# Kernel optimization log

Hardware: AMD Instinct MI355X
Metric: run time of the kernel (lower is better)

## Reference

```python
import jax, jax.numpy as jnp
import numpy as np

N_NODES = 50000
N_EDGES = 800000
D = 128


def _gcn_norm(edge_index, edge_weights, n_nodes):
    # PyG gcn_norm with add_self_loops=True, fill_value=1.0
    src = jnp.concatenate([edge_index[0], jnp.arange(n_nodes)])
    dst = jnp.concatenate([edge_index[1], jnp.arange(n_nodes)])
    w = jnp.concatenate([edge_weights, jnp.ones((n_nodes,), edge_weights.dtype)])
    deg = jax.ops.segment_sum(w, dst, num_segments=n_nodes)
    dinv = jnp.where(deg > 0, jax.lax.rsqrt(deg), 0.0)
    norm = dinv[src] * w * dinv[dst]  # [E + N]
    return src, dst, norm


def _gcn_conv(x, src, dst, norm, W, b, n_nodes):
    h = x @ W                                   # [N, F_out]
    msg = h[src] * norm[:, None]                # gather + scale, [E+N, F_out]
    out = jax.ops.segment_sum(msg, dst, num_segments=n_nodes)
    return out + b


def setup_inputs() -> dict:
    key = jax.random.key(0)
    ks = jax.random.split(key, 12)
    s = 1.0 / np.sqrt(D)
    return {
        "x": jax.random.normal(ks[0], (N_NODES, D), jnp.float32),
        "edge_index": jax.random.randint(ks[1], (2, N_EDGES), 0, N_NODES, jnp.int64),
        "edge_weights": jax.random.uniform(ks[2], (N_EDGES,), jnp.float32),
        "W1": jax.random.normal(ks[3], (D, D), jnp.float32) * s,
        "b1": jnp.zeros((D,), jnp.float32),
        "W2": jax.random.normal(ks[4], (D, D), jnp.float32) * s,
        "b2": jnp.zeros((D,), jnp.float32),
        "W3": jax.random.normal(ks[5], (D, D), jnp.float32) * s,
        "b3": jnp.zeros((D,), jnp.float32),
        "Wl": jax.random.normal(ks[6], (D, D), jnp.float32) * s,
        "bl": jnp.zeros((D,), jnp.float32),
    }


def reference(x, edge_index, edge_weights, W1, b1, W2, b2, W3, b3, Wl, bl):
    n = x.shape[0]
    src, dst, norm = _gcn_norm(edge_index, edge_weights, n)
    h = _gcn_conv(x, src, dst, norm, W1, b1, n)
    h = jax.nn.relu(h)
    h = _gcn_conv(h, src, dst, norm, W2, b2, n)
    h = jax.nn.relu(h)
    h = _gcn_conv(h, src, dst, norm, W3, b3, n)
    # final 'linear' activation entry == nn.Linear(out_size, out_size)
    return h @ Wl + bl
```

## Files before the change

kernel.cpp:

```cpp
#include <hip/hip_runtime.h>
#include <hip/hip_fp16.h>


#define D 128
#define FXS 16777216.0f

typedef __attribute__((ext_vector_type(8))) _Float16 half8;
typedef __attribute__((ext_vector_type(4))) float floatx4;

__global__ __launch_bounds__(256) void k_init(unsigned long long* packed, int N) {
    int i = blockIdx.x * 256 + threadIdx.x;
    if (i < N) packed[i] = 0ull;
}

__global__ __launch_bounds__(256) void k_edge_pass1(const int* __restrict__ dst,
                                                    const float* __restrict__ w,
                                                    unsigned long long* packed,
                                                    int* __restrict__ loc, int E) {
    int e = blockIdx.x * 256 + threadIdx.x;
    if (e < E) {
        int d = dst[e];
        unsigned long long add =
            (1ull << 32) | (unsigned long long)__float2uint_rn(w[e] * FXS);
        unsigned long long old = atomicAdd(&packed[d], add);
        loc[e] = (int)(old >> 32);
    }
}

__global__ __launch_bounds__(256) void k_dinv(const unsigned long long* __restrict__ packed,
                                              float* dinv, int* cnt, int N) {
    int i = blockIdx.x * 256 + threadIdx.x;
    if (i < N) {
        unsigned long long p = packed[i];
        float deg = 1.0f + (float)(unsigned int)(p & 0xffffffffull) * (1.0f / FXS);
        dinv[i] = rsqrtf(deg);
        cnt[i] = (int)(p >> 32);
    }
}

__device__ inline int block_exscan_256(int v) {
    int tid = threadIdx.x;
    int lane = tid & 63, wv = tid >> 6;
    int incl = v;
#pragma unroll
    for (int d = 1; d < 64; d <<= 1) {
        int n = __shfl_up(incl, d, 64);
        if (lane >= d) incl += n;
    }
    __shared__ int wsum[4];
    if (lane == 63) wsum[wv] = incl;
    __syncthreads();
    int woff = 0;
#pragma unroll
    for (int j = 0; j < 4; j++) woff += (j < wv) ? wsum[j] : 0;
    return woff + incl - v;
}

__global__ __launch_bounds__(256) void k_scan_a(const int* __restrict__ cnt,
                                                int* bsum, int N) {
    int i = blockIdx.x * 256 + threadIdx.x;
    int v = (i < N) ? cnt[i] : 0;
#pragma unroll
    for (int d = 32; d; d >>= 1) v += __shfl_down(v, d, 64);
    __shared__ int ws4[4];
    int lane = threadIdx.x & 63, wv = threadIdx.x >> 6;
    if (lane == 0) ws4[wv] = v;
    __syncthreads();
    if (threadIdx.x == 0) bsum[blockIdx.x] = ws4[0] + ws4[1] + ws4[2] + ws4[3];
}

__global__ __launch_bounds__(256) void k_scan_b(const int* __restrict__ bsum,
                                                int* boff, int nb) {
    int tid = threadIdx.x;
    int v = (tid < nb) ? bsum[tid] : 0;
    int ex = block_exscan_256(v);
    if (tid < nb) boff[tid] = ex;
}

__global__ __launch_bounds__(256) void k_scan_c(const int* __restrict__ cnt,
                                                const int* __restrict__ boff,
                                                int* rp, int N, int E) {
    int i = blockIdx.x * 256 + threadIdx.x;
    int v = (i < N) ? cnt[i] : 0;
    int ex = block_exscan_256(v);
    if (i < N) rp[i] = boff[blockIdx.x] + ex;
    if (i == 0) rp[N] = E;
}

__global__ __launch_bounds__(256) void k_fill(const int* __restrict__ ei,
                                              const float* __restrict__ w,
                                              const float* __restrict__ dinv,
                                              const int* __restrict__ rp,
                                              const int* __restrict__ loc,
                                              float2* ev, int E) {
    int e = blockIdx.x * 256 + threadIdx.x;
    if (e < E) {
        int s = ei[e];
        int d = ei[E + e];
        int p = rp[d] + loc[e];
        ev[p] = make_float2(__int_as_float(s), dinv[s] * w[e] * dinv[d]);
    }
}

template <bool A_IS_F32>
__global__ __launch_bounds__(256) void k_gemm_mfma(const void* __restrict__ Aptr,
                                                   const float* __restrict__ W,
                                                   const float* __restrict__ bias,
                                                   float* __restrict__ C32,
                                                   __half* __restrict__ C16, int N) {
    __shared__ _Float16 Wl[128][136];
    int tid = threadIdx.x;

#pragma unroll
    for (int j = 0; j < 64; j++) {
        int e = tid + j * 256;
        int k = e >> 7, n = e & 127;
        Wl[n][k] = (_Float16)W[e];
    }
    __syncthreads();

    int wave = tid >> 6, lane = tid & 63;
    int m = lane & 15, q = lane >> 4;
    int R0 = blockIdx.x * 128 + wave * 32;

    const float*   A32p = (const float*)Aptr;
    const __half*  A16p = (const __half*)Aptr;

    floatx4 acc[2][8];
#pragma unroll
    for (int rt = 0; rt < 2; rt++)
#pragma unroll
        for (int ct = 0; ct < 8; ct++) acc[rt][ct] = (floatx4){0.f, 0.f, 0.f, 0.f};

#pragma unroll
    for (int kk = 0; kk < 4; kk++) {
        half8 a[2];
#pragma unroll
        for (int rt = 0; rt < 2; rt++) {
            int row = R0 + rt * 16 + m;
            half8 t = {0, 0, 0, 0, 0, 0, 0, 0};
            if (row < N) {
                if (A_IS_F32) {
                    const float* p = &A32p[(size_t)row * 128 + kk * 32 + q * 8];
                    float4 f0 = *(const float4*)p;
                    float4 f1 = *(const float4*)(p + 4);
                    t[0] = (_Float16)f0.x; t[1] = (_Float16)f0.y;
                    t[2] = (_Float16)f0.z; t[3] = (_Float16)f0.w;
                    t[4] = (_Float16)f1.x; t[5] = (_Float16)f1.y;
                    t[6] = (_Float16)f1.z; t[7] = (_Float16)f1.w;
                } else {
                    t = *(const half8*)&A16p[(size_t)row * 128 + kk * 32 + q * 8];
                }
            }
            a[rt] = t;
        }
#pragma unroll
        for (int ct = 0; ct < 8; ct++) {
            half8 b = *(const half8*)&Wl[ct * 16 + m][kk * 32 + q * 8];
            acc[0][ct] = __builtin_amdgcn_mfma_f32_16x16x32_f16(a[0], b, acc[0][ct], 0, 0, 0);
            acc[1][ct] = __builtin_amdgcn_mfma_f32_16x16x32_f16(a[1], b, acc[1][ct], 0, 0, 0);
        }
    }

#pragma unroll
    for (int rt = 0; rt < 2; rt++) {
#pragma unroll
        for (int ct = 0; ct < 8; ct++) {
            int col = ct * 16 + m;
            float bcol = (bias != nullptr) ? bias[col] : 0.f;
#pragma unroll
            for (int r = 0; r < 4; r++) {
                int row = R0 + rt * 16 + q * 4 + r;
                if (row < N) {
                    float v = acc[rt][ct][r];
                    if (C16) C16[(size_t)row * 128 + col] = __float2half_rn(v);
                    if (C32) C32[(size_t)row * 128 + col] = v + bcol;
                }
            }
        }
    }
}

__global__ __launch_bounds__(256) void k_agg(const __half* __restrict__ h16,
                                             const int* __restrict__ rp,
                                             const float2* __restrict__ ev,
                                             const float* __restrict__ dinv,
                                             const float* __restrict__ bias,
                                             __half* __restrict__ out16,
                                             int N, int relu) {
    int wave = blockIdx.x * 4 + (threadIdx.x >> 6);
    if (wave >= N) return;
    int lane = threadIdx.x & 63;
    int g = lane >> 4;
    int sl = lane & 15;
    int i = wave;

    float acc[8];
#pragma unroll
    for (int j = 0; j < 8; j++) acc[j] = 0.f;

    int e0 = rp[i], e1 = rp[i + 1];
    int e = e0;

#define GFMA(Q, V)                                                        \
    {                                                                     \
        union { uint4 u; __half2 h2[4]; } U; U.u = (Q);                   \
        float2 f0 = __half22float2(U.h2[0]);                              \
        float2 f1 = __half22float2(U.h2[1]);                              \
        float2 f2 = __half22float2(U.h2[2]);                              \
        float2 f3 = __half22float2(U.h2[3]);                              \
        acc[0] = fmaf(V, f0.x, acc[0]); acc[1] = fmaf(V, f0.y, acc[1]);   \
        acc[2] = fmaf(V, f1.x, acc[2]); acc[3] = fmaf(V, f1.y, acc[3]);   \
        acc[4] = fmaf(V, f2.x, acc[4]); acc[5] = fmaf(V, f2.y, acc[5]);   \
        acc[6] = fmaf(V, f3.x, acc[6]); acc[7] = fmaf(V, f3.y, acc[7]);   \
    }

    for (; e + 16 <= e1; e += 16) {
        float2 pA = ev[e + g];
        float2 pB = ev[e + 4 + g];
        float2 pC = ev[e + 8 + g];
        float2 pD = ev[e + 12 + g];
        uint4 qA = *(const uint4*)&h16[(size_t)__float_as_int(pA.x) * D + sl * 8];
        uint4 qB = *(const uint4*)&h16[(size_t)__float_as_int(pB.x) * D + sl * 8];
        uint4 qC = *(const uint4*)&h16[(size_t)__float_as_int(pC.x) * D + sl * 8];
        uint4 qD = *(const uint4*)&h16[(size_t)__float_as_int(pD.x) * D + sl * 8];
        GFMA(qA, pA.y); GFMA(qB, pB.y); GFMA(qC, pC.y); GFMA(qD, pD.y);
    }
    if (e + 8 <= e1) {
        float2 pA = ev[e + g];
        float2 pB = ev[e + 4 + g];
        uint4 qA = *(const uint4*)&h16[(size_t)__float_as_int(pA.x) * D + sl * 8];
        uint4 qB = *(const uint4*)&h16[(size_t)__float_as_int(pB.x) * D + sl * 8];
        GFMA(qA, pA.y); GFMA(qB, pB.y);
        e += 8;
    }
    if (e + 4 <= e1) {
        float2 pA = ev[e + g];
        uint4 qA = *(const uint4*)&h16[(size_t)__float_as_int(pA.x) * D + sl * 8];
        GFMA(qA, pA.y);
        e += 4;
    }
    if (e + g < e1) {
        float2 pA = ev[e + g];
        uint4 qA = *(const uint4*)&h16[(size_t)__float_as_int(pA.x) * D + sl * 8];
        GFMA(qA, pA.y);
    }
#undef GFMA

#pragma unroll
    for (int j = 0; j < 8; j++) {
        acc[j] += __shfl_xor(acc[j], 16, 64);
        acc[j] += __shfl_xor(acc[j], 32, 64);
    }

    if (g == 0) {
        float di = dinv[i];
        float self = di * di;
        union { uint4 u; __half2 h2[4]; } S;
        S.u = *(const uint4*)&h16[(size_t)i * D + sl * 8];
        float2 s0 = __half22float2(S.h2[0]);
        float2 s1 = __half22float2(S.h2[1]);
        float2 s2 = __half22float2(S.h2[2]);
        float2 s3 = __half22float2(S.h2[3]);
        float4 b0 = *(const float4*)&bias[sl * 8];
        float4 b1 = *(const float4*)&bias[sl * 8 + 4];
        float o[8];
        o[0] = acc[0] + b0.x + self * s0.x;
        o[1] = acc[1] + b0.y + self * s0.y;
        o[2] = acc[2] + b0.z + self * s1.x;
        o[3] = acc[3] + b0.w + self * s1.y;
        o[4] = acc[4] + b1.x + self * s2.x;
        o[5] = acc[5] + b1.y + self * s2.y;
        o[6] = acc[6] + b1.z + self * s3.x;
        o[7] = acc[7] + b1.w + self * s3.y;
        if (relu) {
#pragma unroll
            for (int j = 0; j < 8; j++) o[j] = fmaxf(o[j], 0.f);
        }
        union { uint4 u; __half2 h2[4]; } O;
        O.h2[0] = __float22half2_rn(make_float2(o[0], o[1]));
        O.h2[1] = __float22half2_rn(make_float2(o[2], o[3]));
        O.h2[2] = __float22half2_rn(make_float2(o[4], o[5]));
        O.h2[3] = __float22half2_rn(make_float2(o[6], o[7]));
        *(uint4*)&out16[(size_t)i * D + sl * 8] = O.u;
    }
}

extern "C" void kernel_launch(void* const* d_in, const int* in_sizes, int n_in,
                              void* d_out, int out_size, void* d_ws, size_t ws_size,
                              hipStream_t stream) {
    const float* x  = (const float*)d_in[0];
    const int*   ei = (const int*)d_in[1];
    const float* ew = (const float*)d_in[2];
    const float* W1 = (const float*)d_in[3];
    const float* b1 = (const float*)d_in[4];
    const float* W2 = (const float*)d_in[5];
    const float* b2 = (const float*)d_in[6];
    const float* W3 = (const float*)d_in[7];
    const float* b3 = (const float*)d_in[8];
    const float* Wl = (const float*)d_in[9];
    const float* bl = (const float*)d_in[10];

    int N = in_sizes[0] / D;
    int E = in_sizes[2];

    char* ws = (char*)d_ws;
    size_t off = 0;
    auto alloc = [&](size_t bytes) {
        void* p = ws + off;
        off = (off + bytes + 255) & ~(size_t)255;
        return p;
    };
    unsigned long long* packed = (unsigned long long*)alloc((size_t)N * 8);
    float*  dinv = (float*)alloc((size_t)N * 4);
    int*    cnt  = (int*)  alloc((size_t)N * 4);
    int*    bsum = (int*)  alloc(1024);
    int*    boff = (int*)  alloc(1024);
    int*    rp   = (int*)  alloc((size_t)(N + 1) * 4);
    int*    loc  = (int*)  alloc((size_t)E * 4);
    float2* ev   = (float2*)alloc((size_t)E * 8);
    __half* y16  = (__half*)alloc((size_t)N * D * 2);
    __half* z16  = (__half*)alloc((size_t)N * D * 2);

    int nbN = (N + 255) / 256;
    int nbE = (E + 255) / 256;

    k_init<<<nbN, 256, 0, stream>>>(packed, N);
    k_edge_pass1<<<nbE, 256, 0, stream>>>(ei + E, ew, packed, loc, E);
    k_dinv<<<nbN, 256, 0, stream>>>(packed, dinv, cnt, N);
    k_scan_a<<<nbN, 256, 0, stream>>>(cnt, bsum, N);
    k_scan_b<<<1, 256, 0, stream>>>(bsum, boff, nbN);
    k_scan_c<<<nbN, 256, 0, stream>>>(cnt, boff, rp, N, E);
    k_fill<<<nbE, 256, 0, stream>>>(ei, ew, dinv, rp, loc, ev, E);

    int gg = (N + 127) / 128;
    int ga = (N + 3) / 4;

    k_gemm_mfma<true ><<<gg, 256, 0, stream>>>(x,   W1, nullptr, nullptr, y16, N);
    k_agg<<<ga, 256, 0, stream>>>(y16, rp, ev, dinv, b1, z16, N, 1);
    k_gemm_mfma<false><<<gg, 256, 0, stream>>>(z16, W2, nullptr, nullptr, y16, N);
    k_agg<<<ga, 256, 0, stream>>>(y16, rp, ev, dinv, b2, z16, N, 1);
    k_gemm_mfma<false><<<gg, 256, 0, stream>>>(z16, W3, nullptr, nullptr, y16, N);
    k_agg<<<ga, 256, 0, stream>>>(y16, rp, ev, dinv, b3, z16, N, 0);
    k_gemm_mfma<false><<<gg, 256, 0, stream>>>(z16, Wl, bl, (float*)d_out, nullptr, N);
}
```

Baseline: 309.8 us.

## Pack edges into 32-bit words and fold symmetric normalization into GEMM epilogue

Edge records shrink from an 8-byte (src, norm) pair to a 4-byte word holding a 17-bit source index and a 15-bit quantized weight. The per-edge dinv[s]*dinv[d] factor is factored out: each GEMM scales its output rows by dinv, and aggregation multiplies by dinv of the destination. Degree is now computed from the CSR in a separate kernel, and the count atomics use strided padding instead of a packed 64-bit atomic. This halves edge-list traffic in the three aggregation passes. The cost is weight precision, down to about 15 bits, and a hard limit of 131072 nodes.

After: 305.0 us. Within noise of the previous version (-1.5%).

```diff
diff --git a/kernel.cpp b/kernel.cpp
--- a/kernel.cpp
+++ b/kernel.cpp
@@ -3,38 +3,19 @@
 
 
 #define D 128
-#define FXS 16777216.0f
 
 typedef __attribute__((ext_vector_type(8))) _Float16 half8;
 typedef __attribute__((ext_vector_type(4))) float floatx4;
 
-__global__ __launch_bounds__(256) void k_init(unsigned long long* packed, int N) {
-    int i = blockIdx.x * 256 + threadIdx.x;
-    if (i < N) packed[i] = 0ull;
-}
+#define CNT_STRIDE 16
 
 __global__ __launch_bounds__(256) void k_edge_pass1(const int* __restrict__ dst,
-                                                    const float* __restrict__ w,
-                                                    unsigned long long* packed,
+                                                    unsigned int* __restrict__ cntp,
                                                     int* __restrict__ loc, int E) {
     int e = blockIdx.x * 256 + threadIdx.x;
     if (e < E) {
         int d = dst[e];
-        unsigned long long add =
-            (1ull << 32) | (unsigned long long)__float2uint_rn(w[e] * FXS);
-        unsigned long long old = atomicAdd(&packed[d], add);
-        loc[e] = (int)(old >> 32);
-    }
-}
-
-__global__ __launch_bounds__(256) void k_dinv(const unsigned long long* __restrict__ packed,
-                                              float* dinv, int* cnt, int N) {
-    int i = blockIdx.x * 256 + threadIdx.x;
-    if (i < N) {
-        unsigned long long p = packed[i];
-        float deg = 1.0f + (float)(unsigned int)(p & 0xffffffffull) * (1.0f / FXS);
-        dinv[i] = rsqrtf(deg);
-        cnt[i] = (int)(p >> 32);
+        loc[e] = (int)atomicAdd(&cntp[(size_t)d * CNT_STRIDE], 1u);
     }
 }
 
@@ -56,10 +37,10 @@
     return woff + incl - v;
 }
 
-__global__ __launch_bounds__(256) void k_scan_a(const int* __restrict__ cnt,
+__global__ __launch_bounds__(256) void k_scan_a(const unsigned int* __restrict__ cntp,
                                                 int* bsum, int N) {
     int i = blockIdx.x * 256 + threadIdx.x;
-    int v = (i < N) ? cnt[i] : 0;
+    int v = (i < N) ? (int)cntp[(size_t)i * CNT_STRIDE] : 0;
 #pragma unroll
     for (int d = 32; d; d >>= 1) v += __shfl_down(v, d, 64);
     __shared__ int ws4[4];
@@ -77,11 +58,11 @@
     if (tid < nb) boff[tid] = ex;
 }
 
-__global__ __launch_bounds__(256) void k_scan_c(const int* __restrict__ cnt,
+__global__ __launch_bounds__(256) void k_scan_c(const unsigned int* __restrict__ cntp,
                                                 const int* __restrict__ boff,
                                                 int* rp, int N, int E) {
     int i = blockIdx.x * 256 + threadIdx.x;
-    int v = (i < N) ? cnt[i] : 0;
+    int v = (i < N) ? (int)cntp[(size_t)i * CNT_STRIDE] : 0;
     int ex = block_exscan_256(v);
     if (i < N) rp[i] = boff[blockIdx.x] + ex;
     if (i == 0) rp[N] = E;
@@ -89,22 +70,36 @@
 
 __global__ __launch_bounds__(256) void k_fill(const int* __restrict__ ei,
                                               const float* __restrict__ w,
-                                              const float* __restrict__ dinv,
                                               const int* __restrict__ rp,
                                               const int* __restrict__ loc,
-                                              float2* ev, int E) {
+                                              unsigned int* __restrict__ ev, int E) {
     int e = blockIdx.x * 256 + threadIdx.x;
     if (e < E) {
         int s = ei[e];
         int d = ei[E + e];
         int p = rp[d] + loc[e];
-        ev[p] = make_float2(__int_as_float(s), dinv[s] * w[e] * dinv[d]);
+        unsigned int wq = (unsigned int)__float2uint_rn(w[e] * 32767.0f);
+        ev[p] = (wq << 17) | (unsigned int)s;
+    }
+}
+
+__global__ __launch_bounds__(256) void k_deg(const int* __restrict__ rp,
+                                             const unsigned int* __restrict__ ev,
+                                             float* __restrict__ dinv, int N) {
+    int i = blockIdx.x * 256 + threadIdx.x;
+    if (i < N) {
+        int e0 = rp[i], e1 = rp[i + 1];
+        float s = 0.f;
+        for (int e = e0; e < e1; e++)
+            s += (float)(ev[e] >> 17);
+        dinv[i] = rsqrtf(1.0f + s * (1.0f / 32767.0f));
     }
 }
 
 template <bool A_IS_F32>
 __global__ __launch_bounds__(256) void k_gemm_mfma(const void* __restrict__ Aptr,
                                                    const float* __restrict__ W,
+                                                   const float* __restrict__ dinv,
                                                    const float* __restrict__ bias,
                                                    float* __restrict__ C32,
                                                    __half* __restrict__ C16, int N) {
@@ -123,8 +118,8 @@
     int m = lane & 15, q = lane >> 4;
     int R0 = blockIdx.x * 128 + wave * 32;
 
-    const float*   A32p = (const float*)Aptr;
-    const __half*  A16p = (const __half*)Aptr;
+    const float*  A32p = (const float*)Aptr;
+    const __half* A16p = (const __half*)Aptr;
 
     floatx4 acc[2][8];
 #pragma unroll
@@ -165,25 +160,24 @@
 #pragma unroll
     for (int rt = 0; rt < 2; rt++) {
 #pragma unroll
-        for (int ct = 0; ct < 8; ct++) {
-            int col = ct * 16 + m;
-            float bcol = (bias != nullptr) ? bias[col] : 0.f;
-#pragma unroll
-            for (int r = 0; r < 4; r++) {
-                int row = R0 + rt * 16 + q * 4 + r;
-                if (row < N) {
-                    float v = acc[rt][ct][r];
-                    if (C16) C16[(size_t)row * 128 + col] = __float2half_rn(v);
-                    if (C32) C32[(size_t)row * 128 + col] = v + bcol;
-                }
+        for (int r = 0; r < 4; r++) {
+            int row = R0 + rt * 16 + q * 4 + r;
+            if (row >= N) continue;
+            float dv = (dinv != nullptr) ? dinv[row] : 1.0f;
+#pragma unroll
+            for (int ct = 0; ct < 8; ct++) {
+                int col = ct * 16 + m;
+                float v = acc[rt][ct][r] * dv;
+                if (C16) C16[(size_t)row * 128 + col] = __float2half_rn(v);
+                if (C32) C32[(size_t)row * 128 + col] = v + bias[col];
             }
         }
     }
 }
 
-__global__ __launch_bounds__(256) void k_agg(const __half* __restrict__ h16,
+__global__ __launch_bounds__(256) void k_agg(const __half* __restrict__ y16,
                                              const int* __restrict__ rp,
-                                             const float2* __restrict__ ev,
+                                             const unsigned int* __restrict__ ev,
                                              const float* __restrict__ dinv,
                                              const float* __restrict__ bias,
                                              __half* __restrict__ out16,
@@ -214,37 +208,45 @@
         acc[4] = fmaf(V, f2.x, acc[4]); acc[5] = fmaf(V, f2.y, acc[5]);   \
         acc[6] = fmaf(V, f3.x, acc[6]); acc[7] = fmaf(V, f3.y, acc[7]);   \
     }
+#define UNPK(P, C, V)                                                     \
+    int   C = (int)((P) & 0x1FFFFu);                                      \
+    float V = (float)((P) >> 17) * (1.0f / 32767.0f);
 
     for (; e + 16 <= e1; e += 16) {
-        float2 pA = ev[e + g];
-        float2 pB = ev[e + 4 + g];
-        float2 pC = ev[e + 8 + g];
-        float2 pD = ev[e + 12 + g];
-        uint4 qA = *(const uint4*)&h16[(size_t)__float_as_int(pA.x) * D + sl * 8];
-        uint4 qB = *(const uint4*)&h16[(size_t)__float_as_int(pB.x) * D + sl * 8];
-        uint4 qC = *(const uint4*)&h16[(size_t)__float_as_int(pC.x) * D + sl * 8];
-        uint4 qD = *(const uint4*)&h16[(size_t)__float_as_int(pD.x) * D + sl * 8];
-        GFMA(qA, pA.y); GFMA(qB, pB.y); GFMA(qC, pC.y); GFMA(qD, pD.y);
+        unsigned int pA = ev[e + g];
+        unsigned int pB = ev[e + 4 + g];
+        unsigned int pC = ev[e + 8 + g];
+        unsigned int pD = ev[e + 12 + g];
+        UNPK(pA, cA, vA); UNPK(pB, cB, vB); UNPK(pC, cC, vC); UNPK(pD, cD, vD);
+        uint4 qA = *(const uint4*)&y16[(size_t)cA * D + sl * 8];
+        uint4 qB = *(const uint4*)&y16[(size_t)cB * D + sl * 8];
+        uint4 qC = *(const uint4*)&y16[(size_t)cC * D + sl * 8];
+        uint4 qD = *(const uint4*)&y16[(size_t)cD * D + sl * 8];
+        GFMA(qA, vA); GFMA(qB, vB); GFMA(qC, vC); GFMA(qD, vD);
     }
     if (e + 8 <= e1) {
-        float2 pA = ev[e + g];
-        float2 pB = ev[e + 4 + g];
-        uint4 qA = *(const uint4*)&h16[(size_t)__float_as_int(pA.x) * D + sl * 8];
-        uint4 qB = *(const uint4*)&h16[(size_t)__float_as_int(pB.x) * D + sl * 8];
-        GFMA(qA, pA.y); GFMA(qB, pB.y);
+        unsigned int pA = ev[e + g];
+        unsigned int pB = ev[e + 4 + g];
+        UNPK(pA, cA, vA); UNPK(pB, cB, vB);
+        uint4 qA = *(const uint4*)&y16[(size_t)cA * D + sl * 8];
+        uint4 qB = *(const uint4*)&y16[(size_t)cB * D + sl * 8];
+        GFMA(qA, vA); GFMA(qB, vB);
         e += 8;
     }
     if (e + 4 <= e1) {
-        float2 pA = ev[e + g];
-        uint4 qA = *(const uint4*)&h16[(size_t)__float_as_int(pA.x) * D + sl * 8];
-        GFMA(qA, pA.y);
+        unsigned int pA = ev[e + g];
+        UNPK(pA, cA, vA);
+        uint4 qA = *(const uint4*)&y16[(size_t)cA * D + sl * 8];
+        GFMA(qA, vA);
         e += 4;
     }
     if (e + g < e1) {
-        float2 pA = ev[e + g];
-        uint4 qA = *(const uint4*)&h16[(size_t)__float_as_int(pA.x) * D + sl * 8];
-        GFMA(qA, pA.y);
-    }
+        unsigned int pA = ev[e + g];
+        UNPK(pA, cA, vA);
+        uint4 qA = *(const uint4*)&y16[(size_t)cA * D + sl * 8];
+        GFMA(qA, vA);
+    }
+#undef UNPK
 #undef GFMA
 
 #pragma unroll
@@ -255,9 +257,8 @@
 
     if (g == 0) {
         float di = dinv[i];
-        float self = di * di;
         union { uint4 u; __half2 h2[4]; } S;
-        S.u = *(const uint4*)&h16[(size_t)i * D + sl * 8];
+        S.u = *(const uint4*)&y16[(size_t)i * D + sl * 8];
         float2 s0 = __half22float2(S.h2[0]);
         float2 s1 = __half22float2(S.h2[1]);
         float2 s2 = __half22float2(S.h2[2]);
@@ -265,14 +266,14 @@
         float4 b0 = *(const float4*)&bias[sl * 8];
         float4 b1 = *(const float4*)&bias[sl * 8 + 4];
         float o[8];
-        o[0] = acc[0] + b0.x + self * s0.x;
-        o[1] = acc[1] + b0.y + self * s0.y;
-        o[2] = acc[2] + b0.z + self * s1.x;
-        o[3] = acc[3] + b0.w + self * s1.y;
-        o[4] = acc[4] + b1.x + self * s2.x;
-        o[5] = acc[5] + b1.y + self * s2.y;
-        o[6] = acc[6] + b1.z + self * s3.x;
-        o[7] = acc[7] + b1.w + self * s3.y;
+        o[0] = b0.x + di * (acc[0] + s0.x);
+        o[1] = b0.y + di * (acc[1] + s0.y);
+        o[2] = b0.z + di * (acc[2] + s1.x);
+        o[3] = b0.w + di * (acc[3] + s1.y);
+        o[4] = b1.x + di * (acc[4] + s2.x);
+        o[5] = b1.y + di * (acc[5] + s2.y);
+        o[6] = b1.z + di * (acc[6] + s3.x);
+        o[7] = b1.w + di * (acc[7] + s3.y);
         if (relu) {
 #pragma unroll
             for (int j = 0; j < 8; j++) o[j] = fmaxf(o[j], 0.f);
@@ -311,36 +312,35 @@
         off = (off + bytes + 255) & ~(size_t)255;
         return p;
     };
-    unsigned long long* packed = (unsigned long long*)alloc((size_t)N * 8);
+    unsigned int* cntp = (unsigned int*)alloc((size_t)N * CNT_STRIDE * 4);
     float*  dinv = (float*)alloc((size_t)N * 4);
-    int*    cnt  = (int*)  alloc((size_t)N * 4);
     int*    bsum = (int*)  alloc(1024);
     int*    boff = (int*)  alloc(1024);
     int*    rp   = (int*)  alloc((size_t)(N + 1) * 4);
     int*    loc  = (int*)  alloc((size_t)E * 4);
-    float2* ev   = (float2*)alloc((size_t)E * 8);
+    unsigned int* ev = (unsigned int*)alloc((size_t)E * 4);
     __half* y16  = (__half*)alloc((size_t)N * D * 2);
     __half* z16  = (__half*)alloc((size_t)N * D * 2);
 
     int nbN = (N + 255) / 256;
     int nbE = (E + 255) / 256;
 
-    k_init<<<nbN, 256, 0, stream>>>(packed, N);
-    k_edge_pass1<<<nbE, 256, 0, stream>>>(ei + E, ew, packed, loc, E);
-    k_dinv<<<nbN, 256, 0, stream>>>(packed, dinv, cnt, N);
-    k_scan_a<<<nbN, 256, 0, stream>>>(cnt, bsum, N);
+    hipMemsetAsync(cntp, 0, (size_t)N * CNT_STRIDE * 4, stream);
+    k_edge_pass1<<<nbE, 256, 0, stream>>>(ei + E, cntp, loc, E);
+    k_scan_a<<<nbN, 256, 0, stream>>>(cntp, bsum, N);
     k_scan_b<<<1, 256, 0, stream>>>(bsum, boff, nbN);
-    k_scan_c<<<nbN, 256, 0, stream>>>(cnt, boff, rp, N, E);
-    k_fill<<<nbE, 256, 0, stream>>>(ei, ew, dinv, rp, loc, ev, E);
+    k_scan_c<<<nbN, 256, 0, stream>>>(cntp, boff, rp, N, E);
+    k_fill<<<nbE, 256, 0, stream>>>(ei, ew, rp, loc, ev, E);
+    k_deg<<<nbN, 256, 0, stream>>>(rp, ev, dinv, N);
 
     int gg = (N + 127) / 128;
     int ga = (N + 3) / 4;
 
-    k_gemm_mfma<true ><<<gg, 256, 0, stream>>>(x,   W1, nullptr, nullptr, y16, N);
+    k_gemm_mfma<true ><<<gg, 256, 0, stream>>>(x,   W1, dinv, nullptr, nullptr, y16, N);
     k_agg<<<ga, 256, 0, stream>>>(y16, rp, ev, dinv, b1, z16, N, 1);
-    k_gemm_mfma<false><<<gg, 256, 0, stream>>>(z16, W2, nullptr, nullptr, y16, N);
+    k_gemm_mfma<false><<<gg, 256, 0, stream>>>(z16, W2, dinv, nullptr, nullptr, y16, N);
     k_agg<<<ga, 256, 0, stream>>>(y16, rp, ev, dinv, b2, z16, N, 1);
-    k_gemm_mfma<false><<<gg, 256, 0, stream>>>(z16, W3, nullptr, nullptr, y16, N);
+    k_gemm_mfma<false><<<gg, 256, 0, stream>>>(z16, W3, dinv, nullptr, nullptr, y16, N);
     k_agg<<<ga, 256, 0, stream>>>(y16, rp, ev, dinv, b3, z16, N, 0);
-    k_gemm_mfma<false><<<gg, 256, 0, stream>>>(z16, Wl, bl, (float*)d_out, nullptr, N);
-}
+    k_gemm_mfma<false><<<gg, 256, 0, stream>>>(z16, Wl, nullptr, bl, (float*)d_out, nullptr, N);
+}
```
